# Performance work log

Hardware: AMD Instinct MI355X
Metric: run time of the kernel (lower is better)

## Reference

```python
import jax, jax.numpy as jnp
import numpy as np

DIM = 512; HEADS = 8; DHEAD = 64; INNER = HEADS * DHEAD
T = 9; H = 16; W = 16; KS = 5; KT = 7
SEQ = T * H * W + 1          # 2305 tokens incl. BOS
GH = 48; GW = 48             # axial grid: sqrt(T*H*W) = 48
B = 2


def _nearby_mask_np():
    """Faithful numpy port of generate_nearby_mask(causal=True). True = masked."""
    te = (KT - 1) // 2
    frame = H * W
    S = T * frame
    pad = KS // 2
    tmpl = (np.arange(KS * KS) >= (KS * KS) // 2).reshape(KS, KS)
    mb = np.ones((S, T, H + 2 * pad, W + 2 * pad), dtype=bool)
    for t in range(T):
        for h in range(H):
            for w in range(W):
                i = t * frame + h * W + w
                mb[i, t, h:h + KS, w:w + KS] = tmpl
                mb[i, max(0, t - te):t, h:h + KS, w:w + KS] = False
    mb = mb[:, :, pad:-pad, pad:-pad].reshape(S, S)
    mb = np.roll(mb, -1, axis=0)
    out = np.ones((S + 1, S + 1), dtype=bool)  # pad 1 row/col of True at top-left
    out[1:, 1:] = mb
    out[0, 0] = False
    return out


def setup_inputs() -> dict:
    key = jax.random.key(0)
    ks = jax.random.split(key, 16)
    inp = {
        "x": jax.random.normal(ks[0], (B, SEQ, DIM), jnp.float32),
        "nearby_mask": jnp.asarray(_nearby_mask_np()),
    }
    i = 1
    for l in range(3):
        for nm in ("Wq", "Wk", "Wv", "Wo"):
            inp[f"{nm}{l}"] = jax.random.normal(ks[i], (DIM, INNER), jnp.float32) * 0.02
            i += 1
        inp[f"bo{l}"] = jnp.zeros((DIM,), jnp.float32)
    return inp


def _neg(dt):
    return -jnp.finfo(dt).max


def _axial(x, Wq, Wk, Wv, Wo, bo, typ):
    # type 0: attend along rows (width axis); type 1: attend along columns.
    b = x.shape[0]
    scale = DHEAD ** -0.5
    q, k, v = x @ Wq, x @ Wk, x @ Wv

    def split(t):
        bos = t[:, :1].reshape(b, 1, HEADS, DHEAD).transpose(0, 2, 1, 3)[:, :, None]  # b hd 1 1 d
        img = t[:, 1:].reshape(b, GH, GW, HEADS, DHEAD)
        if typ == 0:
            img = img.transpose(0, 3, 1, 2, 4)  # b hd h w d
            nq = GH
        else:
            img = img.transpose(0, 3, 2, 1, 4)  # b hd w h d
            nq = GW
        bos = jnp.broadcast_to(bos, (b, HEADS, nq, 1, DHEAD))
        return jnp.concatenate([bos, img], axis=3)  # b hd nq (1+len) d

    qs, ks, vs = split(q), split(k), split(v)
    dots = jnp.einsum('bhnid,bhnjd->bhnij', qs, ks) * scale
    L = dots.shape[-1]
    causal = jnp.triu(jnp.ones((L, L), dtype=bool), 1)
    dots = jnp.where(causal, _neg(dots.dtype), dots)
    attn = jax.nn.softmax(dots, axis=-1)
    out = jnp.einsum('bhnij,bhnjd->bhnid', attn, vs)
    out_bos = out[:, :, 0, 0].reshape(b, 1, INNER)
    oi = out[:, :, :, 1:, :]
    if typ == 0:
        oi = oi.transpose(0, 2, 3, 1, 4).reshape(b, GH * GW, INNER)  # b (h w) (hd d)
    else:
        oi = oi.transpose(0, 3, 2, 1, 4).reshape(b, GH * GW, INNER)
    return jnp.concatenate([out_bos, oi], axis=1) @ Wo + bo


def _nearby(x, Wq, Wk, Wv, Wo, bo, mask):
    b, n, _ = x.shape
    scale = DHEAD ** -0.5
    q = (x @ Wq).reshape(b, n, HEADS, DHEAD).transpose(0, 2, 1, 3)
    k = (x @ Wk).reshape(b, n, HEADS, DHEAD).transpose(0, 2, 1, 3)
    v = (x @ Wv).reshape(b, n, HEADS, DHEAD).transpose(0, 2, 1, 3)
    dots = jnp.einsum('bhid,bhjd->bhij', q, k) * scale
    dots = jnp.where(mask, _neg(dots.dtype), dots)
    attn = jax.nn.softmax(dots, axis=-1)
    out = jnp.einsum('bhij,bhjd->bhid', attn, v)
    return out.transpose(0, 2, 1, 3).reshape(b, n, INNER) @ Wo + bo


def reference(x, nearby_mask,
              Wq0, Wk0, Wv0, Wo0, bo0,
              Wq1, Wk1, Wv1, Wo1, bo1,
              Wq2, Wk2, Wv2, Wo2, bo2):
    x = x + _axial(x, Wq0, Wk0, Wv0, Wo0, bo0, 0)   # row axial
    x = x + _axial(x, Wq1, Wk1, Wv1, Wo1, bo1, 1)   # column axial
    x = x + _nearby(x, Wq2, Wk2, Wv2, Wo2, bo2, nearby_mask)  # nearby sparse-mask attn
    return x
```

## Files before the change

kernel.cpp:

```cpp
#include <hip/hip_runtime.h>
#include <hip/hip_bf16.h>

#define SEQ 2305
#define NROWS 4610
#define MPAD 4736
#define DIM 512
#define QKVN 1536

typedef __attribute__((ext_vector_type(8))) short v8s;
typedef __attribute__((ext_vector_type(4))) float v4f;

__device__ __forceinline__ float bf2f(unsigned short u) {
    return __uint_as_float(((unsigned)u) << 16);
}

__device__ __forceinline__ void load_lds16(const void* g, void* l) {
    __builtin_amdgcn_global_load_lds(
        (const __attribute__((address_space(1))) void*)g,
        (__attribute__((address_space(3))) void*)l, 16, 0, 0);
}

struct WPack { const float* p[12]; };

__global__ void prep_inputs(WPack wp, __hip_bfloat16* __restrict__ wqkv,
                            __hip_bfloat16* __restrict__ wo,
                            const float4* __restrict__ xin, float4* __restrict__ xout,
                            __hip_bfloat16* __restrict__ xb, int n4) {
    int tx = threadIdx.x, ty = threadIdx.y;
    int m = blockIdx.z;
    if (m == 12) {
        int tidl = ty * 32 + tx;
        int bid = blockIdx.y * 16 + blockIdx.x;
        for (int i = bid * 256 + tidl; i < n4; i += 65536) {
            float4 v = xin[i];
            xout[i] = v;
            int j = i * 4;
            xb[j + 0] = __float2bfloat16(v.x);
            xb[j + 1] = __float2bfloat16(v.y);
            xb[j + 2] = __float2bfloat16(v.z);
            xb[j + 3] = __float2bfloat16(v.w);
        }
        return;
    }
    __shared__ float tile[32][33];
    const float* src = wp.p[m];
    int l = m >> 2, j = m & 3;
    __hip_bfloat16* dst = (j < 3) ? (wqkv + (size_t)l * QKVN * DIM + (size_t)j * DIM * DIM)
                                  : (wo + (size_t)l * DIM * DIM);
    int bx = blockIdx.x * 32, by = blockIdx.y * 32;
    #pragma unroll
    for (int i = 0; i < 4; i++)
        tile[ty + 8 * i][tx] = src[(size_t)(by + ty + 8 * i) * DIM + bx + tx];
    __syncthreads();
    #pragma unroll
    for (int i = 0; i < 4; i++)
        dst[(size_t)(bx + ty + 8 * i) * DIM + by + tx] = __float2bfloat16(tile[tx][ty + 8 * i]);
}

__global__ __launch_bounds__(256) void gemm_lds(
    const __hip_bfloat16* __restrict__ A, const __hip_bfloat16* __restrict__ Bt,
    float* __restrict__ C, const float* __restrict__ bias, const float* __restrict__ res,
    __hip_bfloat16* __restrict__ Cb, int M, int N) {
    __shared__ short As[2][64 * 32];
    __shared__ short Bs[2][128 * 32];
    const int K = 512;
    int tid = threadIdx.x;
    int wid = tid >> 6, lane = tid & 63;
    int quad = lane >> 4, l16 = lane & 15;
    int bM = blockIdx.x * 64, bN = blockIdx.y * 128;
    int wM = (wid >> 1) * 32, wN = (wid & 1) * 64;

    const short* Ag = (const short*)A;
    const short* Bg = (const short*)Bt;

    int rowS = tid >> 2, cg = tid & 3;
    const short* gA = Ag + (size_t)(bM + rowS) * K + cg * 8;
    const short* gB0 = Bg + (size_t)(bN + rowS) * K + cg * 8;
    const short* gB1 = Bg + (size_t)(bN + 64 + rowS) * K + cg * 8;

    v4f acc[2][4] = {};
    for (int k0 = 0; k0 < K; k0 += 64) {
        #pragma unroll
        for (int s = 0; s < 2; s++) {
            load_lds16(gA + k0 + s * 32, As[s] + wid * 512);
            load_lds16(gB0 + k0 + s * 32, Bs[s] + wid * 512);
            load_lds16(gB1 + k0 + s * 32, Bs[s] + 2048 + wid * 512);
        }
        __syncthreads();
        #pragma unroll
        for (int s = 0; s < 2; s++) {
            v8s af[2], bf[4];
            #pragma unroll
            for (int i = 0; i < 2; i++)
                af[i] = *(const v8s*)(As[s] + (wM + i * 16 + l16) * 32 + quad * 8);
            #pragma unroll
            for (int j = 0; j < 4; j++)
                bf[j] = *(const v8s*)(Bs[s] + (wN + j * 16 + l16) * 32 + quad * 8);
            #pragma unroll
            for (int i = 0; i < 2; i++)
                #pragma unroll
                for (int j = 0; j < 4; j++)
                    acc[i][j] = __builtin_amdgcn_mfma_f32_16x16x32_bf16(af[i], bf[j], acc[i][j], 0, 0, 0);
        }
        __syncthreads();
    }

    #pragma unroll
    for (int i = 0; i < 2; i++) {
        int row = bM + wM + i * 16 + quad * 4;
        #pragma unroll
        for (int j = 0; j < 4; j++) {
            int col = bN + wN + j * 16 + l16;
            #pragma unroll
            for (int r = 0; r < 4; r++) {
                int rr = row + r;
                if (rr < M) {
                    float v = acc[i][j][r];
                    if (bias) v += bias[col];
                    if (res) v += res[(size_t)rr * N + col];
                    size_t idx = (size_t)rr * N + col;
                    if (C) C[idx] = v;
                    if (Cb) Cb[idx] = __float2bfloat16(v);
                }
            }
        }
    }
}

__global__ __launch_bounds__(256) void axial_flash(
    const unsigned short* __restrict__ qkvb, __hip_bfloat16* __restrict__ attn_b, int typ) {
    __shared__ short Ks[64 * 64];
    __shared__ short Vs[64 * 64];
    __shared__ short Ps[64 * 72];
    __shared__ float invl[64];

    int tid = threadIdx.x;
    int wid = tid >> 6, lane = tid & 63;
    int quad = lane >> 4, l16 = lane & 15;
    int n = blockIdx.x;
    int b = blockIdx.y >> 3, h = blockIdx.y & 7;
    size_t rowbase = (size_t)b * SEQ;
    int hoff = h * 64;

    #pragma unroll
    for (int it = 0; it < 2; it++) {
        int linear = it * 256 + tid;
        int slot = linear >> 3;
        int cd = linear & 7;
        int cs = cd ^ (slot & 7);
        int sp = (slot == 0) ? 0
               : (slot <= 48 ? (typ == 0 ? 1 + n * 48 + (slot - 1) : 1 + (slot - 1) * 48 + n) : 0);
        const unsigned short* srcK = qkvb + (rowbase + sp) * QKVN + hoff + 512 + cs * 8;
        load_lds16(srcK, Ks + it * 2048 + wid * 512 + lane * 8);
        const unsigned short* srcV = qkvb + (rowbase + sp) * QKVN + hoff + 1024 + cd * 8;
        load_lds16(srcV, Vs + it * 2048 + wid * 512 + lane * 8);
    }

    int qi = wid * 16 + l16;
    int sp_q = (qi >= 1 && qi <= 48)
             ? (typ == 0 ? 1 + n * 48 + (qi - 1) : 1 + (qi - 1) * 48 + n) : 0;
    const unsigned short* qptr = qkvb + (rowbase + sp_q) * QKVN + hoff + quad * 8;
    v8s qa0 = *(const v8s*)qptr;
    v8s qa1 = *(const v8s*)(qptr + 32);

    __syncthreads();

    if (n == 0 && tid < 64) {
        attn_b[rowbase * DIM + hoff + tid] =
            __float2bfloat16(bf2f(qkvb[rowbase * QKVN + hoff + 1024 + tid]));
    }

    v4f st[4];
    #pragma unroll
    for (int kt = 0; kt < 4; kt++) {
        int slot = kt * 16 + l16;
        int s7 = slot & 7;
        v8s blo = *(const v8s*)(Ks + slot * 64 + ((quad ^ s7) * 8));
        v8s bhi = *(const v8s*)(Ks + slot * 64 + (((4 + quad) ^ s7) * 8));
        v4f a = {};
        a = __builtin_amdgcn_mfma_f32_16x16x32_bf16(qa0, blo, a, 0, 0, 0);
        a = __builtin_amdgcn_mfma_f32_16x16x32_bf16(qa1, bhi, a, 0, 0, 0);
        st[kt] = a;
    }

    const float NEG = -3.0e38f;
    float sv[4][4];
    float pm[4] = {NEG, NEG, NEG, NEG};
    #pragma unroll
    for (int kt = 0; kt < 4; kt++) {
        int j = kt * 16 + l16;
        #pragma unroll
        for (int r = 0; r < 4; r++) {
            int i = wid * 16 + quad * 4 + r;
            bool ok = (i >= 1) && (i <= 48) && (j <= i);
            float v = ok ? st[kt][r] * 0.125f : NEG;
            sv[kt][r] = v;
            pm[r] = fmaxf(pm[r], v);
        }
    }
    #pragma unroll
    for (int r = 0; r < 4; r++)
        for (int o = 1; o < 16; o <<= 1) pm[r] = fmaxf(pm[r], __shfl_xor(pm[r], o));

    float ps[4] = {0.f, 0.f, 0.f, 0.f};
    #pragma unroll
    for (int kt = 0; kt < 4; kt++) {
        int j = kt * 16 + l16;
        #pragma unroll
        for (int r = 0; r < 4; r++) {
            float e = __expf(sv[kt][r] - pm[r]);
            ps[r] += e;
            Ps[(wid * 16 + quad * 4 + r) * 72 + j] = (short)__bfloat16_as_ushort(__float2bfloat16(e));
        }
    }
    #pragma unroll
    for (int r = 0; r < 4; r++)
        for (int o = 1; o < 16; o <<= 1) ps[r] += __shfl_xor(ps[r], o);
    if (l16 == 0) {
        #pragma unroll
        for (int r = 0; r < 4; r++)
            invl[wid * 16 + quad * 4 + r] = 1.0f / ps[r];
    }
    __syncthreads();

    #pragma unroll
    for (int qt = 0; qt < 4; qt++) {
        v4f oc = {};
        #pragma unroll
        for (int kc = 0; kc < 2; kc++) {
            v8s pa = *(const v8s*)(Ps + (qt * 16 + l16) * 72 + kc * 32 + quad * 8);
            v8s bfr;
            #pragma unroll
            for (int jj = 0; jj < 8; jj++)
                bfr[jj] = Vs[(kc * 32 + quad * 8 + jj) * 64 + wid * 16 + l16];
            oc = __builtin_amdgcn_mfma_f32_16x16x32_bf16(pa, bfr, oc, 0, 0, 0);
        }
        #pragma unroll
        for (int r = 0; r < 4; r++) {
            int i = qt * 16 + quad * 4 + r;
            if (i >= 1 && i <= 48) {
                int sp = typ == 0 ? 1 + n * 48 + (i - 1) : 1 + (i - 1) * 48 + n;
                attn_b[(rowbase + sp) * DIM + hoff + wid * 16 + l16] =
                    __float2bfloat16(oc[r] * invl[i]);
            }
        }
    }
}

__global__ void meanv_part(const unsigned short* __restrict__ qkvb, float* __restrict__ part) {
    int b = blockIdx.x >> 4, ch = blockIdx.x & 15;
    int col = blockIdx.y * 256 + threadIdx.x;
    int j0 = ch * 145, j1 = j0 + 145;
    if (j1 > SEQ) j1 = SEQ;
    const unsigned short* p = qkvb + (size_t)b * SEQ * QKVN + 1024 + col;
    float s = 0.f;
    #pragma unroll 4
    for (int j = j0; j < j1; j++) s += bf2f(p[(size_t)j * QKVN]);
    part[((size_t)(b * 16 + ch)) * 512 + col] = s;
}
__global__ void meanv_fold(const float* __restrict__ part,
                           const unsigned short* __restrict__ qkvb,
                           __hip_bfloat16* __restrict__ attn_b) {
    int b = blockIdx.x;
    int col = blockIdx.y * 256 + threadIdx.x;
    float s = 0.f;
    #pragma unroll
    for (int ch = 0; ch < 16; ch++) s += part[((size_t)(b * 16 + ch)) * 512 + col];
    attn_b[((size_t)b * SEQ + 2304) * DIM + col] = __float2bfloat16(s * (1.0f / 2305.0f));
    attn_b[((size_t)b * SEQ) * DIM + col] =
        __float2bfloat16(bf2f(qkvb[(size_t)b * SEQ * QKVN + 1024 + col]));
}

__global__ __launch_bounds__(256) void nearby_flash(
    const unsigned short* __restrict__ qkvb, __hip_bfloat16* __restrict__ attn_b) {
    __shared__ short Vs[128 * 64];
    __shared__ __hip_bfloat16 Ps[16 * 264];
    __shared__ float redm[16 * 4];
    __shared__ float reds[16 * 4];

    int tid = threadIdx.x;
    int wid = tid >> 6, lane = tid & 63;
    int quad = lane >> 4, l16 = lane & 15;

    int idx = blockIdx.x;
    int bh = idx & 15;
    int tile = idx >> 4;
    int b = bh >> 3, h = bh & 7;
    int t = tile >> 4;
    int sxy = tile & 15;
    int hh0 = (sxy >> 2) * 4, ww0 = (sxy & 3) * 4;
    int nf = (t < 3 ? t : 3) + 1;
    int t0 = t - (nf - 1);
    size_t rowbase = (size_t)b * SEQ;
    int hoff = h * 64;

    auto slot_kp = [&](int slot) -> int {
        int f = slot >> 6, uy = (slot >> 3) & 7, ux = slot & 7;
        int kh = hh0 - 2 + uy, kw = ww0 - 2 + ux;
        int kt = t0 + f;
        bool ok = (kh >= 0) && (kh < 16) && (kw >= 0) && (kw < 16) && (f < nf);
        return ok ? (kt * 256 + kh * 16 + kw + 1) : 0;
    };

    int qp_f = t * 256 + (hh0 + (l16 >> 2)) * 16 + (ww0 + (l16 & 3));
    const unsigned short* qptr = qkvb + (rowbase + qp_f) * QKVN + hoff + quad * 8;
    v8s qa0 = *(const v8s*)qptr;
    v8s qa1 = *(const v8s*)(qptr + 32);

    v8s kb_lo[4], kb_hi[4];
    #pragma unroll
    for (int k = 0; k < 4; k++) {
        int slot = (wid * 4 + k) * 16 + l16;
        int kp = slot_kp(slot);
        const unsigned short* kr = qkvb + (rowbase + kp) * QKVN + hoff + 512;
        kb_lo[k] = *(const v8s*)(kr + quad * 8);
        kb_hi[k] = *(const v8s*)(kr + 32 + quad * 8);
    }

    #pragma unroll
    for (int it = 0; it < 4; it++) {
        int linear = it * 256 + tid;
        int slot = linear >> 3;
        int cd = linear & 7;
        int cs = cd ^ ((slot >> 3) & 7);
        int kp = slot_kp(slot);
        const unsigned short* src = qkvb + (rowbase + kp) * QKVN + hoff + 1024 + cs * 8;
        load_lds16(src, Vs + it * 2048 + wid * 512 + lane * 8);
    }

    v4f st[4];
    #pragma unroll
    for (int k = 0; k < 4; k++) {
        v4f a = {};
        a = __builtin_amdgcn_mfma_f32_16x16x32_bf16(qa0, kb_lo[k], a, 0, 0, 0);
        a = __builtin_amdgcn_mfma_f32_16x16x32_bf16(qa1, kb_hi[k], a, 0, 0, 0);
        st[k] = a;
    }

    const float NEG = -3.0e38f;
    float sv[4][4];
    float pm[4] = {NEG, NEG, NEG, NEG};
    #pragma unroll
    for (int k = 0; k < 4; k++) {
        int slot = (wid * 4 + k) * 16 + l16;
        int f = slot >> 6, uy = (slot >> 3) & 7, ux = slot & 7;
        int kh = hh0 - 2 + uy, kw = ww0 - 2 + ux;
        bool okb = (kh >= 0) && (kh < 16) && (kw >= 0) && (kw < 16) && (f < nf);
        int dyp2 = uy - quad;
        bool oky = okb && (dyp2 >= 0) && (dyp2 <= 4);
        #pragma unroll
        for (int r = 0; r < 4; r++) {
            int dxp2 = ux - r;
            bool ok = oky && (dxp2 >= 0) && (dxp2 <= 4);
            if (f == nf - 1) ok = ok && (dyp2 * 5 + dxp2 < 12);
            float v = ok ? st[k][r] * 0.125f : NEG;
            sv[k][r] = v;
            pm[r] = fmaxf(pm[r], v);
        }
    }
    #pragma unroll
    for (int r = 0; r < 4; r++)
        for (int o = 1; o < 16; o <<= 1) pm[r] = fmaxf(pm[r], __shfl_xor(pm[r], o));
    if (l16 == 0) {
        #pragma unroll
        for (int r = 0; r < 4; r++) redm[(quad * 4 + r) * 4 + wid] = pm[r];
    }
    __syncthreads();

    float rm[4];
    #pragma unroll
    for (int r = 0; r < 4; r++) {
        int row = (quad * 4 + r) * 4;
        rm[r] = fmaxf(fmaxf(redm[row], redm[row + 1]), fmaxf(redm[row + 2], redm[row + 3]));
    }

    float ps[4] = {0.f, 0.f, 0.f, 0.f};
    #pragma unroll
    for (int k = 0; k < 4; k++) {
        int slot = (wid * 4 + k) * 16 + l16;
        #pragma unroll
        for (int r = 0; r < 4; r++) {
            float e = __expf(sv[k][r] - rm[r]);
            ps[r] += e;
            Ps[(quad * 4 + r) * 264 + slot] = __float2bfloat16(e);
        }
    }
    #pragma unroll
    for (int r = 0; r < 4; r++)
        for (int o = 1; o < 16; o <<= 1) ps[r] += __shfl_xor(ps[r], o);
    if (l16 == 0) {
        #pragma unroll
        for (int r = 0; r < 4; r++) reds[(quad * 4 + r) * 4 + wid] = ps[r];
    }
    __syncthreads();

    float inv[4];
    #pragma unroll
    for (int r = 0; r < 4; r++) {
        int row = (quad * 4 + r) * 4;
        float d = reds[row] + reds[row + 1] + reds[row + 2] + reds[row + 3];
        inv[r] = 1.0f / d;
    }

    int dcol = wid * 16 + l16;
    int c_r = dcol >> 3, d7 = dcol & 7;
    v4f oc = {};
    #pragma unroll
    for (int kc = 0; kc < 4; kc++) {
        v8s pa = *(const v8s*)((const short*)Ps + l16 * 264 + kc * 32 + quad * 8);
        v8s bf;
        #pragma unroll
        for (int j = 0; j < 8; j++) {
            int slot = kc * 32 + quad * 8 + j;
            int key = (slot >> 3) & 7;
            bf[j] = Vs[(slot & 127) * 64 + ((c_r ^ key) * 8) + d7];
        }
        oc = __builtin_amdgcn_mfma_f32_16x16x32_bf16(pa, bf, oc, 0, 0, 0);
    }
    __syncthreads();

    #pragma unroll
    for (int it = 0; it < 4; it++) {
        int linear = 1024 + it * 256 + tid;
        int slot = linear >> 3;
        int cd = linear & 7;
        int cs = cd ^ ((slot >> 3) & 7);
        int kp = slot_kp(slot);
        const unsigned short* src = qkvb + (rowbase + kp) * QKVN + hoff + 1024 + cs * 8;
        load_lds16(src, Vs + it * 2048 + wid * 512 + lane * 8);
    }
    __syncthreads();

    #pragma unroll
    for (int kc = 4; kc < 8; kc++) {
        v8s pa = *(const v8s*)((const short*)Ps + l16 * 264 + kc * 32 + quad * 8);
        v8s bf;
        #pragma unroll
        for (int j = 0; j < 8; j++) {
            int slot = kc * 32 + quad * 8 + j;
            int key = (slot >> 3) & 7;
            bf[j] = Vs[(slot & 127) * 64 + ((c_r ^ key) * 8) + d7];
        }
        oc = __builtin_amdgcn_mfma_f32_16x16x32_bf16(pa, bf, oc, 0, 0, 0);
    }

    #pragma unroll
    for (int r = 0; r < 4; r++) {
        int qp = t * 256 + (hh0 + quad) * 16 + (ww0 + r);
        if (qp != 0) {
            attn_b[(rowbase + qp) * DIM + hoff + dcol] =
                __float2bfloat16(oc[r] * inv[r]);
        }
    }
}

extern "C" void kernel_launch(void* const* d_in, const int* in_sizes, int n_in,
                              void* d_out, int out_size, void* d_ws, size_t ws_size,
                              hipStream_t stream) {
    const float* x = (const float*)d_in[0];
    float* xcur = (float*)d_out;

    char* ws = (char*)d_ws;
    size_t off = 0;
    auto alloc = [&](size_t bytes) -> void* {
        void* p = ws + off;
        off = (off + bytes + 255) & ~(size_t)255;
        return p;
    };
    __hip_bfloat16* wqkv  = (__hip_bfloat16*)alloc((size_t)3 * QKVN * DIM * 2);
    __hip_bfloat16* wo    = (__hip_bfloat16*)alloc((size_t)3 * DIM * DIM * 2);
    __hip_bfloat16* xb    = (__hip_bfloat16*)alloc((size_t)MPAD * DIM * 2);
    __hip_bfloat16* attnb = (__hip_bfloat16*)alloc((size_t)MPAD * DIM * 2);
    float* part           = (float*)alloc((size_t)2 * 16 * 512 * 4);
    __hip_bfloat16* qkvb  = (__hip_bfloat16*)alloc((size_t)NROWS * QKVN * 2);

    const int nElem = NROWS * DIM;
    const int n4 = nElem / 4;

    WPack wp;
    for (int l = 0; l < 3; l++)
        for (int j = 0; j < 4; j++)
            wp.p[l * 4 + j] = (const float*)d_in[2 + l * 5 + j];
    prep_inputs<<<dim3(16, 16, 13), dim3(32, 8), 0, stream>>>(
        wp, wqkv, wo, (const float4*)x, (float4*)xcur, xb, n4);

    for (int l = 0; l < 3; l++) {
        gemm_lds<<<dim3(MPAD / 64, QKVN / 128), 256, 0, stream>>>(
            xb, wqkv + (size_t)l * QKVN * DIM, nullptr, nullptr, nullptr, qkvb, NROWS, QKVN);
        if (l < 2) {
            axial_flash<<<dim3(48, 16), 256, 0, stream>>>((const unsigned short*)qkvb, attnb, l);
        } else {
            meanv_part<<<dim3(32, 2), 256, 0, stream>>>((const unsigned short*)qkvb, part);
            meanv_fold<<<dim3(2, 2), 256, 0, stream>>>(part, (const unsigned short*)qkvb, attnb);
            nearby_flash<<<2304, 256, 0, stream>>>((const unsigned short*)qkvb, attnb);
        }
        const float* bo = (const float*)d_in[6 + l * 5];
        gemm_lds<<<dim3(MPAD / 64, DIM / 128), 256, 0, stream>>>(
            attnb, wo + (size_t)l * DIM * DIM, xcur, bo, xcur, xb, NROWS, DIM);
    }
}
```

Before: 290.6 us.

## Keep residual stream in bf16 and load GEMM A operand directly to registers

The fp32 residual copy is dropped. The residual is read back from the bf16 activation buffer, and the fp32 output is written only in the final layer, which cuts fp32 global reads and writes per output projection. The GEMM also stops staging the A tile through LDS: each wave loads its A fragments straight from global memory into registers. This lowers precision of the residual path (bf16 accumulation across layers) and relies on A reads being cached well. In-place reading and writing of xb is used when the GEMM's output equals its residual source.

Measured after the change: 311.2 us. +7.1%, slower.

```diff
diff --git a/kernel.cpp b/kernel.cpp
--- a/kernel.cpp
+++ b/kernel.cpp
@@ -24,7 +24,7 @@
 
 __global__ void prep_inputs(WPack wp, __hip_bfloat16* __restrict__ wqkv,
                             __hip_bfloat16* __restrict__ wo,
-                            const float4* __restrict__ xin, float4* __restrict__ xout,
+                            const float4* __restrict__ xin,
                             __hip_bfloat16* __restrict__ xb, int n4) {
     int tx = threadIdx.x, ty = threadIdx.y;
     int m = blockIdx.z;
@@ -33,7 +33,6 @@
         int bid = blockIdx.y * 16 + blockIdx.x;
         for (int i = bid * 256 + tidl; i < n4; i += 65536) {
             float4 v = xin[i];
-            xout[i] = v;
             int j = i * 4;
             xb[j + 0] = __float2bfloat16(v.x);
             xb[j + 1] = __float2bfloat16(v.y);
@@ -59,9 +58,9 @@
 
 __global__ __launch_bounds__(256) void gemm_lds(
     const __hip_bfloat16* __restrict__ A, const __hip_bfloat16* __restrict__ Bt,
-    float* __restrict__ C, const float* __restrict__ bias, const float* __restrict__ res,
-    __hip_bfloat16* __restrict__ Cb, int M, int N) {
-    __shared__ short As[2][64 * 32];
+    float* __restrict__ C, const float* __restrict__ bias,
+    const __hip_bfloat16* __restrict__ resb, __hip_bfloat16* __restrict__ Cb,
+    int M, int N) {
     __shared__ short Bs[2][128 * 32];
     const int K = 512;
     int tid = threadIdx.x;
@@ -74,25 +73,28 @@
     const short* Bg = (const short*)Bt;
 
     int rowS = tid >> 2, cg = tid & 3;
-    const short* gA = Ag + (size_t)(bM + rowS) * K + cg * 8;
     const short* gB0 = Bg + (size_t)(bN + rowS) * K + cg * 8;
     const short* gB1 = Bg + (size_t)(bN + 64 + rowS) * K + cg * 8;
 
+    const short* aptr0 = Ag + (size_t)(bM + wM + l16) * K + quad * 8;
+    const short* aptr1 = Ag + (size_t)(bM + wM + 16 + l16) * K + quad * 8;
+
     v4f acc[2][4] = {};
     for (int k0 = 0; k0 < K; k0 += 64) {
+        v8s af[2][2];
+        af[0][0] = *(const v8s*)(aptr0 + k0);
+        af[1][0] = *(const v8s*)(aptr1 + k0);
+        af[0][1] = *(const v8s*)(aptr0 + k0 + 32);
+        af[1][1] = *(const v8s*)(aptr1 + k0 + 32);
         #pragma unroll
         for (int s = 0; s < 2; s++) {
-            load_lds16(gA + k0 + s * 32, As[s] + wid * 512);
             load_lds16(gB0 + k0 + s * 32, Bs[s] + wid * 512);
             load_lds16(gB1 + k0 + s * 32, Bs[s] + 2048 + wid * 512);
         }
         __syncthreads();
         #pragma unroll
         for (int s = 0; s < 2; s++) {
-            v8s af[2], bf[4];
-            #pragma unroll
-            for (int i = 0; i < 2; i++)
-                af[i] = *(const v8s*)(As[s] + (wM + i * 16 + l16) * 32 + quad * 8);
+            v8s bf[4];
             #pragma unroll
             for (int j = 0; j < 4; j++)
                 bf[j] = *(const v8s*)(Bs[s] + (wN + j * 16 + l16) * 32 + quad * 8);
@@ -100,11 +102,12 @@
             for (int i = 0; i < 2; i++)
                 #pragma unroll
                 for (int j = 0; j < 4; j++)
-                    acc[i][j] = __builtin_amdgcn_mfma_f32_16x16x32_bf16(af[i], bf[j], acc[i][j], 0, 0, 0);
+                    acc[i][j] = __builtin_amdgcn_mfma_f32_16x16x32_bf16(af[i][s], bf[j], acc[i][j], 0, 0, 0);
         }
         __syncthreads();
     }
 
+    const unsigned short* resu = (const unsigned short*)resb;
     #pragma unroll
     for (int i = 0; i < 2; i++) {
         int row = bM + wM + i * 16 + quad * 4;
@@ -117,8 +120,8 @@
                 if (rr < M) {
                     float v = acc[i][j][r];
                     if (bias) v += bias[col];
-                    if (res) v += res[(size_t)rr * N + col];
                     size_t idx = (size_t)rr * N + col;
+                    if (resu) v += bf2f(resu[idx]);
                     if (C) C[idx] = v;
                     if (Cb) Cb[idx] = __float2bfloat16(v);
                 }
@@ -482,7 +485,7 @@
         for (int j = 0; j < 4; j++)
             wp.p[l * 4 + j] = (const float*)d_in[2 + l * 5 + j];
     prep_inputs<<<dim3(16, 16, 13), dim3(32, 8), 0, stream>>>(
-        wp, wqkv, wo, (const float4*)x, (float4*)xcur, xb, n4);
+        wp, wqkv, wo, (const float4*)x, xb, n4);
 
     for (int l = 0; l < 3; l++) {
         gemm_lds<<<dim3(MPAD / 64, QKVN / 128), 256, 0, stream>>>(
@@ -495,7 +498,12 @@
             nearby_flash<<<2304, 256, 0, stream>>>((const unsigned short*)qkvb, attnb);
         }
         const float* bo = (const float*)d_in[6 + l * 5];
-        gemm_lds<<<dim3(MPAD / 64, DIM / 128), 256, 0, stream>>>(
-            attnb, wo + (size_t)l * DIM * DIM, xcur, bo, xcur, xb, NROWS, DIM);
-    }
-}
+        if (l < 2) {
+            gemm_lds<<<dim3(MPAD / 64, DIM / 128), 256, 0, stream>>>(
+                attnb, wo + (size_t)l * DIM * DIM, nullptr, bo, xb, xb, NROWS, DIM);
+        } else {
+            gemm_lds<<<dim3(MPAD / 64, DIM / 128), 256, 0, stream>>>(
+                attnb, wo + (size_t)l * DIM * DIM, xcur, bo, xb, nullptr, NROWS, DIM);
+        }
+    }
+}
```
